# Kernel optimization log

Measured on AMD Instinct MI355X. Metric: run time of the kernel, lower is better.

The kernel has to match this reference:

```python
import jax, jax.numpy as jnp
import numpy as np

NUM_HEADS = 8
EMBED_DIM = 512
HEAD_SIZE = EMBED_DIM // NUM_HEADS
B, S = 4, 2048


def setup_inputs() -> dict:
    key = jax.random.key(0)
    ks = jax.random.split(key, 9)
    scale = 1.0 / np.sqrt(HEAD_SIZE)
    return {
        "values": jax.random.normal(ks[0], (B, S, EMBED_DIM), jnp.float32),
        "keys": jax.random.normal(ks[1], (B, S, EMBED_DIM), jnp.float32),
        "query": jax.random.normal(ks[2], (B, S, EMBED_DIM), jnp.float32),
        "mask": jax.random.randint(ks[3], (B, S), 0, 2, jnp.int32),
        # per-head projection weights, nn.Linear convention: y = x @ W.T, W is [out,in]
        "Wv": jax.random.normal(ks[4], (HEAD_SIZE, HEAD_SIZE), jnp.float32) * scale,
        "Wk": jax.random.normal(ks[5], (HEAD_SIZE, HEAD_SIZE), jnp.float32) * scale,
        "Wq": jax.random.normal(ks[6], (HEAD_SIZE, HEAD_SIZE), jnp.float32) * scale,
        "Wo": jax.random.normal(ks[7], (EMBED_DIM, EMBED_DIM), jnp.float32) * (1.0 / np.sqrt(EMBED_DIM)),
        "bo": jax.random.normal(ks[8], (EMBED_DIM,), jnp.float32) * 0.01,
    }


def reference(values, keys, query, mask, Wv, Wk, Wq, Wo, bo):
    b, s, e = query.shape
    h, d = NUM_HEADS, HEAD_SIZE
    # reshape to heads, then shared per-head linear (no bias): x @ W.T
    v = jnp.einsum("bkhd,ed->bkhe", values.reshape(b, s, h, d), Wv)
    k = jnp.einsum("bkhd,ed->bkhe", keys.reshape(b, s, h, d), Wk)
    q = jnp.einsum("bqhd,ed->bqhe", query.reshape(b, s, h, d), Wq)
    # scores [b,h,q,k]
    energy = jnp.einsum("bqhd,bkhd->bhqk", q, k)
    energy = jnp.where(mask[:, None, None, :] == 0, jnp.float32(-1e20), energy)
    # NOTE: original scales by sqrt(embed_dim), not sqrt(head_size)
    attention = jax.nn.softmax(energy / np.sqrt(e).astype(np.float32), axis=3)
    out = jnp.einsum("bhqk,bkhd->bqhd", attention, v).reshape(b, s, e)
    out = out @ Wo.T + bo
    return out, attention
```

## Files before the change

### kernel.cpp

```cpp
#include <hip/hip_runtime.h>
#include <hip/hip_bf16.h>

#define Bn 4
#define Sn 2048
#define Hn 8
#define Dn 64
#define En 512

typedef __attribute__((ext_vector_type(8))) short short8v;
typedef __attribute__((ext_vector_type(4))) float float4v;

__device__ __forceinline__ short f2bf(float x){
    __hip_bfloat16 h = __float2bfloat16(x);
    return *reinterpret_cast<short*>(&h);
}
__device__ __forceinline__ float bf2f(short s){
    union { unsigned int u; float f; } c;
    c.u = ((unsigned int)(unsigned short)s) << 16;
    return c.f;
}

__global__ __launch_bounds__(256) void wo_cvt_kernel(const float* __restrict__ Wo,
                                                     short* __restrict__ Wob){
    int i = (blockIdx.x * 256 + threadIdx.x) * 4;
    float4 v = *(const float4*)(Wo + i);
    short4 o;
    o.x = f2bf(v.x); o.y = f2bf(v.y); o.z = f2bf(v.z); o.w = f2bf(v.w);
    *(short4*)(Wob + i) = o;
}

__global__ __launch_bounds__(256) void proj_kernel(
    const float* __restrict__ values, const float* __restrict__ keys, const float* __restrict__ query,
    const float* __restrict__ Wv, const float* __restrict__ Wk, const float* __restrict__ Wq,
    short* __restrict__ Qp, short* __restrict__ Kp, short* __restrict__ Vt)
{
    const int sel = blockIdx.z;
    const float* X = (sel == 0) ? values : ((sel == 1) ? keys : query);
    const float* W = (sel == 0) ? Wv : ((sel == 1) ? Wk : Wq);
    const int bh = blockIdx.y;
    const int b = bh >> 3, h = bh & 7;
    const int s0 = blockIdx.x * 64;
    const int wave = threadIdx.x >> 6;
    const int lane = threadIdx.x & 63;
    const int l16 = lane & 15, quad = lane >> 4;

    short8v bw[4][2];
    #pragma unroll
    for (int t = 0; t < 4; t++){
      #pragma unroll
      for (int st = 0; st < 2; st++){
        const float* wp = W + (t*16 + l16)*64 + st*32 + quad*8;
        float4 w0 = *(const float4*)(wp);
        float4 w1 = *(const float4*)(wp + 4);
        short8v f;
        f[0]=f2bf(w0.x); f[1]=f2bf(w0.y); f[2]=f2bf(w0.z); f[3]=f2bf(w0.w);
        f[4]=f2bf(w1.x); f[5]=f2bf(w1.y); f[6]=f2bf(w1.z); f[7]=f2bf(w1.w);
        bw[t][st] = f;
      }
    }

    const int row = s0 + wave*16 + l16;
    short8v fa[2];
    #pragma unroll
    for (int st = 0; st < 2; st++){
        const float* xp = X + ((size_t)b*Sn + row)*En + h*Dn + st*32 + quad*8;
        float4 x0 = *(const float4*)(xp);
        float4 x1 = *(const float4*)(xp + 4);
        short8v f;
        f[0]=f2bf(x0.x); f[1]=f2bf(x0.y); f[2]=f2bf(x0.z); f[3]=f2bf(x0.w);
        f[4]=f2bf(x1.x); f[5]=f2bf(x1.y); f[6]=f2bf(x1.z); f[7]=f2bf(x1.w);
        fa[st] = f;
    }

    const int rbase = s0 + wave*16 + quad*4;
    if (sel == 0){
        #pragma unroll
        for (int t = 0; t < 4; t++){
            float4v a = {0.f,0.f,0.f,0.f};
            a = __builtin_amdgcn_mfma_f32_16x16x32_bf16(fa[0], bw[t][0], a, 0,0,0);
            a = __builtin_amdgcn_mfma_f32_16x16x32_bf16(fa[1], bw[t][1], a, 0,0,0);
            int e = t*16 + l16;
            short4 pk;
            pk.x = f2bf(a[0]); pk.y = f2bf(a[1]); pk.z = f2bf(a[2]); pk.w = f2bf(a[3]);
            *(short4*)(Vt + ((size_t)bh*Dn + e)*Sn + rbase) = pk;
        }
    } else {
        short* dst = (sel == 1) ? Kp : Qp;
        #pragma unroll
        for (int t = 0; t < 4; t++){
            float4v a = {0.f,0.f,0.f,0.f};
            a = __builtin_amdgcn_mfma_f32_16x16x32_bf16(fa[0], bw[t][0], a, 0,0,0);
            a = __builtin_amdgcn_mfma_f32_16x16x32_bf16(fa[1], bw[t][1], a, 0,0,0);
            int e = t*16 + l16;
            #pragma unroll
            for (int r = 0; r < 4; r++)
                dst[((size_t)bh*Sn + rbase + r)*Dn + e] = f2bf(a[r]);
        }
    }
}

__global__ __launch_bounds__(256) void attn_kernel(
    const short* __restrict__ Qp, const short* __restrict__ Kp, const short* __restrict__ Vt,
    const int* __restrict__ mask, float* __restrict__ attn, short* __restrict__ Obf)
{
    __shared__ short sc[16][2056];
    __shared__ float wsum[4][16];
    __shared__ float vinv[16];

    const int qt = blockIdx.x, h = blockIdx.y, b = blockIdx.z;
    const int bh = b*Hn + h;
    const int tid = threadIdx.x;
    const int wave = tid >> 6, lane = tid & 63;
    const int l16 = lane & 15, quad = lane >> 4;
    const int q0 = qt * 16;

    const short* Qbase = Qp + (size_t)bh*Sn*Dn;
    const short* Kbase = Kp + (size_t)bh*Sn*Dn;
    const short* Vbase = Vt + (size_t)bh*Dn*Sn;

    short8v qa0 = *(const short8v*)(Qbase + (q0 + l16)*Dn + quad*8);
    short8v qa1 = *(const short8v*)(Qbase + (q0 + l16)*Dn + 32 + quad*8);

    const float SCALE = 0.0441941738241592f;
    float rs0=0.f, rs1=0.f, rs2=0.f, rs3=0.f;
    const int kw = wave * 512;
    const int km = b*Sn;
    for (int t = 0; t < 32; t++){
        const int k0 = kw + t*16;
        short8v kb0 = *(const short8v*)(Kbase + (k0 + l16)*Dn + quad*8);
        short8v kb1 = *(const short8v*)(Kbase + (k0 + l16)*Dn + 32 + quad*8);
        float4v a = {0.f,0.f,0.f,0.f};
        a = __builtin_amdgcn_mfma_f32_16x16x32_bf16(qa0, kb0, a, 0,0,0);
        a = __builtin_amdgcn_mfma_f32_16x16x32_bf16(qa1, kb1, a, 0,0,0);
        const int mk = mask[km + k0 + l16];
        const int col = k0 + l16;
        float p0 = (mk != 0) ? __expf(a[0]*SCALE) : 0.f;
        float p1 = (mk != 0) ? __expf(a[1]*SCALE) : 0.f;
        float p2 = (mk != 0) ? __expf(a[2]*SCALE) : 0.f;
        float p3 = (mk != 0) ? __expf(a[3]*SCALE) : 0.f;
        rs0 += p0; rs1 += p1; rs2 += p2; rs3 += p3;
        sc[quad*4 + 0][col] = f2bf(p0);
        sc[quad*4 + 1][col] = f2bf(p1);
        sc[quad*4 + 2][col] = f2bf(p2);
        sc[quad*4 + 3][col] = f2bf(p3);
    }
    #pragma unroll
    for (int off = 1; off < 16; off <<= 1){
        rs0 += __shfl_xor(rs0, off);
        rs1 += __shfl_xor(rs1, off);
        rs2 += __shfl_xor(rs2, off);
        rs3 += __shfl_xor(rs3, off);
    }
    if (l16 == 0){
        wsum[wave][quad*4 + 0] = rs0;
        wsum[wave][quad*4 + 1] = rs1;
        wsum[wave][quad*4 + 2] = rs2;
        wsum[wave][quad*4 + 3] = rs3;
    }
    __syncthreads();
    if (tid < 16){
        float s = wsum[0][tid] + wsum[1][tid] + wsum[2][tid] + wsum[3][tid];
        vinv[tid] = (s > 0.f) ? 1.f/s : 0.f;
    }
    __syncthreads();

    float* arow = attn + (size_t)bh*Sn*Sn + (size_t)q0*Sn;
    for (int row = 0; row < 16; row++){
        const float sr = vinv[row];
        short8v v8 = *(const short8v*)(&sc[row][tid*8]);
        float4v o0, o1;
        o0[0]=bf2f(v8[0])*sr; o0[1]=bf2f(v8[1])*sr; o0[2]=bf2f(v8[2])*sr; o0[3]=bf2f(v8[3])*sr;
        o1[0]=bf2f(v8[4])*sr; o1[1]=bf2f(v8[5])*sr; o1[2]=bf2f(v8[6])*sr; o1[3]=bf2f(v8[7])*sr;
        float* dst = arow + (size_t)row*Sn + tid*8;
        __builtin_nontemporal_store(o0, (float4v*)dst);
        __builtin_nontemporal_store(o1, (float4v*)(dst + 4));
    }

    float4v oacc0 = {0.f,0.f,0.f,0.f}, oacc1 = {0.f,0.f,0.f,0.f},
            oacc2 = {0.f,0.f,0.f,0.f}, oacc3 = {0.f,0.f,0.f,0.f};
    for (int ks = 0; ks < 16; ks++){
        const int kb = kw + ks*32 + quad*8;
        short8v pa  = *(const short8v*)(&sc[l16][kb]);
        short8v vb0 = *(const short8v*)(Vbase + (size_t)( 0 + l16)*Sn + kb);
        short8v vb1 = *(const short8v*)(Vbase + (size_t)(16 + l16)*Sn + kb);
        short8v vb2 = *(const short8v*)(Vbase + (size_t)(32 + l16)*Sn + kb);
        short8v vb3 = *(const short8v*)(Vbase + (size_t)(48 + l16)*Sn + kb);
        oacc0 = __builtin_amdgcn_mfma_f32_16x16x32_bf16(pa, vb0, oacc0, 0,0,0);
        oacc1 = __builtin_amdgcn_mfma_f32_16x16x32_bf16(pa, vb1, oacc1, 0,0,0);
        oacc2 = __builtin_amdgcn_mfma_f32_16x16x32_bf16(pa, vb2, oacc2, 0,0,0);
        oacc3 = __builtin_amdgcn_mfma_f32_16x16x32_bf16(pa, vb3, oacc3, 0,0,0);
    }
    __syncthreads();
    float* osc = (float*)&sc[0][0];
    {
        const int rb = quad*4;
        #pragma unroll
        for (int r = 0; r < 4; r++){
            osc[wave*1024 + (rb + r)*64 +  0 + l16] = oacc0[r];
            osc[wave*1024 + (rb + r)*64 + 16 + l16] = oacc1[r];
            osc[wave*1024 + (rb + r)*64 + 32 + l16] = oacc2[r];
            osc[wave*1024 + (rb + r)*64 + 48 + l16] = oacc3[r];
        }
    }
    __syncthreads();
    #pragma unroll
    for (int i = 0; i < 4; i++){
        const int id = tid + i*256;
        const int row = id >> 6, d = id & 63;
        float v = osc[id] + osc[1024 + id] + osc[2048 + id] + osc[3072 + id];
        v *= vinv[row];
        Obf[((size_t)b*Sn + q0 + row)*En + h*Dn + d] = f2bf(v);
    }
}

__global__ __launch_bounds__(256) void outproj_kernel(
    const short* __restrict__ Obf, const short* __restrict__ Wob,
    const float* __restrict__ bo, float* __restrict__ out)
{
    const int nt = blockIdx.x;
    const int mt = blockIdx.y;
    const int wave = threadIdx.x >> 6, lane = threadIdx.x & 63;
    const int l16 = lane & 15, quad = lane >> 4;
    const int m0 = mt*64 + wave*16;
    const int n0 = nt*64;

    float4v acc0 = {0.f,0.f,0.f,0.f}, acc1 = {0.f,0.f,0.f,0.f},
            acc2 = {0.f,0.f,0.f,0.f}, acc3 = {0.f,0.f,0.f,0.f};
    for (int ks = 0; ks < 16; ks++){
        const int kb = ks*32 + quad*8;
        short8v af = *(const short8v*)(Obf + (size_t)(m0 + l16)*En + kb);
        short8v b0 = *(const short8v*)(Wob + (size_t)(n0 +  0 + l16)*En + kb);
        short8v b1 = *(const short8v*)(Wob + (size_t)(n0 + 16 + l16)*En + kb);
        short8v b2 = *(const short8v*)(Wob + (size_t)(n0 + 32 + l16)*En + kb);
        short8v b3 = *(const short8v*)(Wob + (size_t)(n0 + 48 + l16)*En + kb);
        acc0 = __builtin_amdgcn_mfma_f32_16x16x32_bf16(af, b0, acc0, 0,0,0);
        acc1 = __builtin_amdgcn_mfma_f32_16x16x32_bf16(af, b1, acc1, 0,0,0);
        acc2 = __builtin_amdgcn_mfma_f32_16x16x32_bf16(af, b2, acc2, 0,0,0);
        acc3 = __builtin_amdgcn_mfma_f32_16x16x32_bf16(af, b3, acc3, 0,0,0);
    }
    #pragma unroll
    for (int t = 0; t < 4; t++){
        float4v a = (t==0)?acc0:((t==1)?acc1:((t==2)?acc2:acc3));
        const int e = n0 + t*16 + l16;
        const float bias = bo[e];
        #pragma unroll
        for (int r = 0; r < 4; r++)
            out[(size_t)(m0 + quad*4 + r)*En + e] = a[r] + bias;
    }
}

extern "C" void kernel_launch(void* const* d_in, const int* in_sizes, int n_in,
                              void* d_out, int out_size, void* d_ws, size_t ws_size,
                              hipStream_t stream)
{
    const float* values = (const float*)d_in[0];
    const float* keys   = (const float*)d_in[1];
    const float* query  = (const float*)d_in[2];
    const int*   mask   = (const int*)d_in[3];
    const float* Wv = (const float*)d_in[4];
    const float* Wk = (const float*)d_in[5];
    const float* Wq = (const float*)d_in[6];
    const float* Wo = (const float*)d_in[7];
    const float* bo = (const float*)d_in[8];

    float* out  = (float*)d_out;
    float* attn = out + (size_t)Bn*Sn*En;

    short* Qp  = (short*)d_ws;
    short* Kp  = Qp + (size_t)Bn*Hn*Sn*Dn;
    short* Vt  = Kp + (size_t)Bn*Hn*Sn*Dn;
    short* Obf = Vt + (size_t)Bn*Hn*Sn*Dn;
    short* Wob = Obf + (size_t)Bn*Sn*En;

    wo_cvt_kernel<<<dim3((En*En)/1024), 256, 0, stream>>>(Wo, Wob);
    proj_kernel<<<dim3(Sn/64, Bn*Hn, 3), 256, 0, stream>>>(values, keys, query, Wv, Wk, Wq, Qp, Kp, Vt);
    attn_kernel<<<dim3(Sn/16, Hn, Bn), 256, 0, stream>>>(Qp, Kp, Vt, mask, attn, Obf);
    outproj_kernel<<<dim3(En/64, (Bn*Sn)/64), 256, 0, stream>>>(Obf, Wob, bo, out);
}
```

Measured before the change: 859.2 us.

## Recompute QK in a second pass to shrink the LDS score buffer

The attention kernel now makes two passes over K. The first pass computes only the softmax row sums. The second pass recomputes the QK scores in slabs of 128 keys per wave, staging them in a small per-wave LDS tile. That tile feeds both the normalized attention-matrix store and the PV MFMA. This cuts the shared-memory footprint from a full 16x2048 bf16 score row buffer to about 17KB, so more blocks can be resident per CU to hide the latency of the large attention write. The cost is twice the QK MFMA and exp work, plus re-reading K from cache.

New measurement: 908.7 us. 5.8% more time.

```diff
diff --git a/kernel.cpp b/kernel.cpp
--- a/kernel.cpp
+++ b/kernel.cpp
@@ -103,7 +103,7 @@
     const short* __restrict__ Qp, const short* __restrict__ Kp, const short* __restrict__ Vt,
     const int* __restrict__ mask, float* __restrict__ attn, short* __restrict__ Obf)
 {
-    __shared__ short sc[16][2056];
+    __shared__ short sc[4][16][136];
     __shared__ float wsum[4][16];
     __shared__ float vinv[16];
 
@@ -117,45 +117,42 @@
     const short* Qbase = Qp + (size_t)bh*Sn*Dn;
     const short* Kbase = Kp + (size_t)bh*Sn*Dn;
     const short* Vbase = Vt + (size_t)bh*Dn*Sn;
+    const int* mrow = mask + b*Sn;
 
     short8v qa0 = *(const short8v*)(Qbase + (q0 + l16)*Dn + quad*8);
     short8v qa1 = *(const short8v*)(Qbase + (q0 + l16)*Dn + 32 + quad*8);
 
     const float SCALE = 0.0441941738241592f;
+
     float rs0=0.f, rs1=0.f, rs2=0.f, rs3=0.f;
-    const int kw = wave * 512;
-    const int km = b*Sn;
-    for (int t = 0; t < 32; t++){
-        const int k0 = kw + t*16;
-        short8v kb0 = *(const short8v*)(Kbase + (k0 + l16)*Dn + quad*8);
-        short8v kb1 = *(const short8v*)(Kbase + (k0 + l16)*Dn + 32 + quad*8);
-        float4v a = {0.f,0.f,0.f,0.f};
-        a = __builtin_amdgcn_mfma_f32_16x16x32_bf16(qa0, kb0, a, 0,0,0);
-        a = __builtin_amdgcn_mfma_f32_16x16x32_bf16(qa1, kb1, a, 0,0,0);
-        const int mk = mask[km + k0 + l16];
-        const int col = k0 + l16;
-        float p0 = (mk != 0) ? __expf(a[0]*SCALE) : 0.f;
-        float p1 = (mk != 0) ? __expf(a[1]*SCALE) : 0.f;
-        float p2 = (mk != 0) ? __expf(a[2]*SCALE) : 0.f;
-        float p3 = (mk != 0) ? __expf(a[3]*SCALE) : 0.f;
-        rs0 += p0; rs1 += p1; rs2 += p2; rs3 += p3;
-        sc[quad*4 + 0][col] = f2bf(p0);
-        sc[quad*4 + 1][col] = f2bf(p1);
-        sc[quad*4 + 2][col] = f2bf(p2);
-        sc[quad*4 + 3][col] = f2bf(p3);
-    }
-    #pragma unroll
-    for (int off = 1; off < 16; off <<= 1){
-        rs0 += __shfl_xor(rs0, off);
-        rs1 += __shfl_xor(rs1, off);
-        rs2 += __shfl_xor(rs2, off);
-        rs3 += __shfl_xor(rs3, off);
-    }
-    if (l16 == 0){
-        wsum[wave][quad*4 + 0] = rs0;
-        wsum[wave][quad*4 + 1] = rs1;
-        wsum[wave][quad*4 + 2] = rs2;
-        wsum[wave][quad*4 + 3] = rs3;
+    {
+        const int kw = wave * 512;
+        for (int t = 0; t < 32; t++){
+            const int k0 = kw + t*16;
+            short8v kb0 = *(const short8v*)(Kbase + (k0 + l16)*Dn + quad*8);
+            short8v kb1 = *(const short8v*)(Kbase + (k0 + l16)*Dn + 32 + quad*8);
+            float4v a = {0.f,0.f,0.f,0.f};
+            a = __builtin_amdgcn_mfma_f32_16x16x32_bf16(qa0, kb0, a, 0,0,0);
+            a = __builtin_amdgcn_mfma_f32_16x16x32_bf16(qa1, kb1, a, 0,0,0);
+            const int mk = mrow[k0 + l16];
+            rs0 += (mk != 0) ? __expf(a[0]*SCALE) : 0.f;
+            rs1 += (mk != 0) ? __expf(a[1]*SCALE) : 0.f;
+            rs2 += (mk != 0) ? __expf(a[2]*SCALE) : 0.f;
+            rs3 += (mk != 0) ? __expf(a[3]*SCALE) : 0.f;
+        }
+        #pragma unroll
+        for (int off = 1; off < 16; off <<= 1){
+            rs0 += __shfl_xor(rs0, off);
+            rs1 += __shfl_xor(rs1, off);
+            rs2 += __shfl_xor(rs2, off);
+            rs3 += __shfl_xor(rs3, off);
+        }
+        if (l16 == 0){
+            wsum[wave][quad*4 + 0] = rs0;
+            wsum[wave][quad*4 + 1] = rs1;
+            wsum[wave][quad*4 + 2] = rs2;
+            wsum[wave][quad*4 + 3] = rs3;
+        }
     }
     __syncthreads();
     if (tid < 16){
@@ -164,42 +161,71 @@
     }
     __syncthreads();
 
-    float* arow = attn + (size_t)bh*Sn*Sn + (size_t)q0*Sn;
-    for (int row = 0; row < 16; row++){
-        const float sr = vinv[row];
-        short8v v8 = *(const short8v*)(&sc[row][tid*8]);
-        float4v o0, o1;
-        o0[0]=bf2f(v8[0])*sr; o0[1]=bf2f(v8[1])*sr; o0[2]=bf2f(v8[2])*sr; o0[3]=bf2f(v8[3])*sr;
-        o1[0]=bf2f(v8[4])*sr; o1[1]=bf2f(v8[5])*sr; o1[2]=bf2f(v8[6])*sr; o1[3]=bf2f(v8[7])*sr;
-        float* dst = arow + (size_t)row*Sn + tid*8;
-        __builtin_nontemporal_store(o0, (float4v*)dst);
-        __builtin_nontemporal_store(o1, (float4v*)(dst + 4));
-    }
-
     float4v oacc0 = {0.f,0.f,0.f,0.f}, oacc1 = {0.f,0.f,0.f,0.f},
             oacc2 = {0.f,0.f,0.f,0.f}, oacc3 = {0.f,0.f,0.f,0.f};
-    for (int ks = 0; ks < 16; ks++){
-        const int kb = kw + ks*32 + quad*8;
-        short8v pa  = *(const short8v*)(&sc[l16][kb]);
-        short8v vb0 = *(const short8v*)(Vbase + (size_t)( 0 + l16)*Sn + kb);
-        short8v vb1 = *(const short8v*)(Vbase + (size_t)(16 + l16)*Sn + kb);
-        short8v vb2 = *(const short8v*)(Vbase + (size_t)(32 + l16)*Sn + kb);
-        short8v vb3 = *(const short8v*)(Vbase + (size_t)(48 + l16)*Sn + kb);
-        oacc0 = __builtin_amdgcn_mfma_f32_16x16x32_bf16(pa, vb0, oacc0, 0,0,0);
-        oacc1 = __builtin_amdgcn_mfma_f32_16x16x32_bf16(pa, vb1, oacc1, 0,0,0);
-        oacc2 = __builtin_amdgcn_mfma_f32_16x16x32_bf16(pa, vb2, oacc2, 0,0,0);
-        oacc3 = __builtin_amdgcn_mfma_f32_16x16x32_bf16(pa, vb3, oacc3, 0,0,0);
-    }
+    short (*scw)[136] = sc[wave];
+    float* arow = attn + (size_t)bh*Sn*Sn + (size_t)q0*Sn;
+
+    for (int slab = 0; slab < 4; slab++){
+        const int kband = slab*512 + wave*128;
+
+        #pragma unroll
+        for (int t = 0; t < 8; t++){
+            const int k0 = kband + t*16;
+            short8v kb0 = *(const short8v*)(Kbase + (k0 + l16)*Dn + quad*8);
+            short8v kb1 = *(const short8v*)(Kbase + (k0 + l16)*Dn + 32 + quad*8);
+            float4v a = {0.f,0.f,0.f,0.f};
+            a = __builtin_amdgcn_mfma_f32_16x16x32_bf16(qa0, kb0, a, 0,0,0);
+            a = __builtin_amdgcn_mfma_f32_16x16x32_bf16(qa1, kb1, a, 0,0,0);
+            const int mk = mrow[k0 + l16];
+            const int col = t*16 + l16;
+            float p0 = (mk != 0) ? __expf(a[0]*SCALE) : 0.f;
+            float p1 = (mk != 0) ? __expf(a[1]*SCALE) : 0.f;
+            float p2 = (mk != 0) ? __expf(a[2]*SCALE) : 0.f;
+            float p3 = (mk != 0) ? __expf(a[3]*SCALE) : 0.f;
+            scw[quad*4 + 0][col] = f2bf(p0);
+            scw[quad*4 + 1][col] = f2bf(p1);
+            scw[quad*4 + 2][col] = f2bf(p2);
+            scw[quad*4 + 3][col] = f2bf(p3);
+        }
+
+        #pragma unroll
+        for (int it = 0; it < 8; it++){
+            const int row = it*2 + (lane >> 5);
+            const int c = (lane & 31) * 4;
+            short4 s4 = *(const short4*)(&scw[row][c]);
+            const float sr = vinv[row];
+            float4v o;
+            o[0] = bf2f(s4.x)*sr; o[1] = bf2f(s4.y)*sr;
+            o[2] = bf2f(s4.z)*sr; o[3] = bf2f(s4.w)*sr;
+            __builtin_nontemporal_store(o, (float4v*)(arow + (size_t)row*Sn + kband + c));
+        }
+
+        #pragma unroll
+        for (int ks = 0; ks < 4; ks++){
+            const int kc = kband + ks*32 + quad*8;
+            short8v pa  = *(const short8v*)(&scw[l16][ks*32 + quad*8]);
+            short8v vb0 = *(const short8v*)(Vbase + (size_t)( 0 + l16)*Sn + kc);
+            short8v vb1 = *(const short8v*)(Vbase + (size_t)(16 + l16)*Sn + kc);
+            short8v vb2 = *(const short8v*)(Vbase + (size_t)(32 + l16)*Sn + kc);
+            short8v vb3 = *(const short8v*)(Vbase + (size_t)(48 + l16)*Sn + kc);
+            oacc0 = __builtin_amdgcn_mfma_f32_16x16x32_bf16(pa, vb0, oacc0, 0,0,0);
+            oacc1 = __builtin_amdgcn_mfma_f32_16x16x32_bf16(pa, vb1, oacc1, 0,0,0);
+            oacc2 = __builtin_amdgcn_mfma_f32_16x16x32_bf16(pa, vb2, oacc2, 0,0,0);
+            oacc3 = __builtin_amdgcn_mfma_f32_16x16x32_bf16(pa, vb3, oacc3, 0,0,0);
+        }
+    }
+
     __syncthreads();
-    float* osc = (float*)&sc[0][0];
+    float* osc = (float*)&sc[0][0][0];
     {
-        const int rb = quad*4;
         #pragma unroll
         for (int r = 0; r < 4; r++){
-            osc[wave*1024 + (rb + r)*64 +  0 + l16] = oacc0[r];
-            osc[wave*1024 + (rb + r)*64 + 16 + l16] = oacc1[r];
-            osc[wave*1024 + (rb + r)*64 + 32 + l16] = oacc2[r];
-            osc[wave*1024 + (rb + r)*64 + 48 + l16] = oacc3[r];
+            const int q = quad*4 + r;
+            osc[wave*1024 + q*64 +  0 + l16] = oacc0[r];
+            osc[wave*1024 + q*64 + 16 + l16] = oacc1[r];
+            osc[wave*1024 + q*64 + 32 + l16] = oacc2[r];
+            osc[wave*1024 + q*64 + 48 + l16] = oacc3[r];
         }
     }
     __syncthreads();
```
